# Kernel tuning notes

Measured on AMD Instinct MI355X. Metric: run time of the kernel, lower is better.

## Reference

```python
import jax, jax.numpy as jnp
import numpy as np

B, L, D, H, NE, M, NP, C, F2 = 2, 1024, 768, 12, 42, 8, 1722, 97, 256


def setup_inputs() -> dict:
    key = jax.random.key(0)
    ks = jax.random.split(key, 12)
    s = 0.02
    sequence_output = jax.random.normal(ks[0], (B, L, D), jnp.float32)
    attention = jax.random.uniform(ks[1], (B, H, L, L), jnp.float32)
    mention_idx = jax.random.randint(ks[2], (B, NE, M), 0, L)
    mention_mask = jax.random.randint(ks[3], (B, NE, M), 0, 2).at[:, :, 0].set(1)
    hts = jax.random.randint(ks[4], (B, NP, 2), 0, NE)
    return dict(
        sequence_output=sequence_output, attention=attention,
        mention_idx=mention_idx, mention_mask=mention_mask, hts=hts,
        W_lin=jax.random.normal(ks[5], (D, 3)) * s, b_lin=jnp.zeros((3,)),
        W_seg=jax.random.normal(ks[6], (3, F2)) * s, b_seg=jnp.zeros((F2,)),
        W_head=jax.random.normal(ks[7], (D, F2)) * s, b_head=jnp.zeros((F2,)),
        W_tail=jax.random.normal(ks[8], (D, F2)) * s, b_tail=jnp.zeros((F2,)),
        W_bil=jax.random.normal(ks[9], (C, F2, F2)) * s, b_bil=jnp.zeros((C,)),
    )


def reference(sequence_output, attention, mention_idx, mention_mask, hts,
              W_lin, b_lin, W_seg, b_seg, W_head, b_head, W_tail, b_tail,
              W_bil, b_bil):
    b_, l_, d_ = sequence_output.shape
    h_ = attention.shape[1]
    ne, m_ = mention_idx.shape[1:]
    NEG = jnp.asarray(-1e30, sequence_output.dtype)
    msk = mention_mask.astype(sequence_output.dtype)  # [B,NE,M]

    bidx = jnp.arange(b_)[:, None, None]
    # --- get_hrt: per-entity mention gather + logsumexp pool / mean pool ---
    ment_emb = sequence_output[bidx, mention_idx]              # [B,NE,M,D]
    ent_emb = jax.nn.logsumexp(jnp.where(msk[..., None] > 0, ment_emb, NEG), axis=2)  # [B,NE,D]
    ment_att = attention[bidx, :, mention_idx]                 # [B,NE,M,H,L]
    ent_att = (ment_att * msk[..., None, None]).sum(2) / msk.sum(2)[..., None, None]  # [B,NE,H,L]

    b2 = jnp.arange(b_)[:, None]
    hs = ent_emb[b2, hts[..., 0]]                              # [B,NP,D]
    ts = ent_emb[b2, hts[..., 1]]

    # --- get_channel_map: all ne*ne pair attention-weighted context ---
    hi = jnp.repeat(jnp.arange(ne), ne)
    ti = jnp.tile(jnp.arange(ne), ne)
    h_att = ent_att[:, hi]                                     # [B,NE*NE,H,L]
    t_att = ent_att[:, ti]
    ht_att = jnp.einsum('bphl,bphl->bpl', h_att, t_att) / h_   # mean over heads
    ht_att = ht_att / (ht_att.sum(-1, keepdims=True) + 1e-5)
    rs = jnp.einsum('bld,bpl->bpd', sequence_output, ht_att)   # [B,NE*NE,D]
    feature_map = rs.reshape(b_, ne, ne, d_)

    # self.linear (D->3) then segmentation net (stand-in: 1x1 conv 3->F2 + relu)
    attn_input = feature_map @ W_lin + b_lin                   # [B,NE,NE,3]
    attn_map = jax.nn.relu(attn_input @ W_seg + b_seg)         # [B,NE,NE,F2]

    # --- get_ht: gather pair features ---
    h_t = attn_map[b2, hts[..., 0], hts[..., 1]]               # [B,NP,F2]
    hs = jnp.tanh(hs @ W_head + b_head + h_t)
    ts = jnp.tanh(ts @ W_tail + b_tail + h_t)
    logits = jnp.einsum('bpi,oij,bpj->bpo', hs, W_bil, ts) + b_bil
    return logits.reshape(-1, logits.shape[-1])               # [B*NP, C]
```

## Files before the change

### kernel.cpp

```cpp
#include <hip/hip_runtime.h>
#include <hip/hip_bf16.h>
#include <math.h>

constexpr int BB = 2;
constexpr int LL = 1024;
constexpr int DD = 768;
constexpr int HH = 12;
constexpr int NEz = 42;
constexpr int MM = 8;
constexpr int NPp = 1722;
constexpr int CC = 97;
constexpr int FF = 256;
constexpr int PAIRS = NEz * NEz;
constexpr int TOTAL = BB * NPp;
constexpr int PT64 = (TOTAL + 63) / 64;

typedef float f32x4 __attribute__((ext_vector_type(4)));
typedef short bf16x8 __attribute__((ext_vector_type(8)));

__global__ void k_seqw(const float* __restrict__ seq, const float* __restrict__ Wl,
                       float* __restrict__ seqW) {
    int bl = blockIdx.x;
    int lane = threadIdx.x;
    const float* row = seq + (size_t)bl * DD;
    float a0 = 0.f, a1 = 0.f, a2 = 0.f;
    for (int d = lane; d < DD; d += 64) {
        float v = row[d];
        a0 += v * Wl[d * 3 + 0];
        a1 += v * Wl[d * 3 + 1];
        a2 += v * Wl[d * 3 + 2];
    }
    for (int off = 32; off; off >>= 1) {
        a0 += __shfl_down(a0, off);
        a1 += __shfl_down(a1, off);
        a2 += __shfl_down(a2, off);
    }
    if (lane == 0) {
        seqW[bl * 3 + 0] = a0;
        seqW[bl * 3 + 1] = a1;
        seqW[bl * 3 + 2] = a2;
    }
}

__global__ void k_ent_emb(const float* __restrict__ seq, const int* __restrict__ midx,
                          const int* __restrict__ mmask, float* __restrict__ ent_emb) {
    int be = blockIdx.x;
    int b = be / NEz;
    int tid = threadIdx.x;
    int idx[MM], msk[MM];
#pragma unroll
    for (int m = 0; m < MM; ++m) {
        idx[m] = midx[be * MM + m];
        msk[m] = mmask[be * MM + m];
    }
    const float* sb = seq + (size_t)b * LL * DD;
    for (int d = tid; d < DD; d += 256) {
        float v[MM];
        float mx = -1e30f;
#pragma unroll
        for (int m = 0; m < MM; ++m) {
            v[m] = msk[m] ? sb[(size_t)idx[m] * DD + d] : -1e30f;
            mx = fmaxf(mx, v[m]);
        }
        float s = 0.f;
#pragma unroll
        for (int m = 0; m < MM; ++m) s += expf(v[m] - mx);
        ent_emb[(size_t)be * DD + d] = mx + logf(s);
    }
}

__global__ void k_ent_att(const float* __restrict__ att, const int* __restrict__ midx,
                          const int* __restrict__ mmask, float* __restrict__ ea) {
    int beh = blockIdx.x;
    int h = beh % HH;
    int be = beh / HH;
    int b = be / NEz;
    int tid = threadIdx.x;
    int idx[MM], msk[MM];
    float msum = 0.f;
#pragma unroll
    for (int m = 0; m < MM; ++m) {
        idx[m] = midx[be * MM + m];
        msk[m] = mmask[be * MM + m];
        msum += (float)msk[m];
    }
    float inv = 1.f / msum;
    const float* ab = att + ((size_t)b * HH + h) * LL * LL;
#pragma unroll
    for (int li = 0; li < 4; ++li) {
        int l = tid + li * 256;
        float acc = 0.f;
#pragma unroll
        for (int m = 0; m < MM; ++m)
            if (msk[m]) acc += ab[(size_t)idx[m] * LL + l];
        ea[(size_t)beh * LL + l] = acc * inv;
    }
}

__global__ void k_pair(const float* __restrict__ ea, const float* __restrict__ seqW,
                       const float* __restrict__ Wseg, const float* __restrict__ bseg,
                       const float* __restrict__ blin, float* __restrict__ am) {
    int bp = blockIdx.x;
    int b = bp / PAIRS;
    int p = bp % PAIRS;
    int e1 = p / NEz, e2 = p % NEz;
    int tid = threadIdx.x;
    int lane = tid & 63, wid = tid >> 6;

    const float* ea1 = ea + ((size_t)(b * NEz + e1)) * HH * LL;
    const float* ea2 = ea + ((size_t)(b * NEz + e2)) * HH * LL;

    float myht[4];
    float lsum = 0.f;
#pragma unroll
    for (int li = 0; li < 4; ++li) {
        int l = tid + li * 256;
        float acc = 0.f;
#pragma unroll
        for (int h = 0; h < HH; ++h) acc += ea1[h * LL + l] * ea2[h * LL + l];
        acc *= (1.0f / HH);
        myht[li] = acc;
        lsum += acc;
    }
    __shared__ float red4[4];
    __shared__ float redz[3][4];
    for (int off = 32; off; off >>= 1) lsum += __shfl_down(lsum, off);
    if (lane == 0) red4[wid] = lsum;
    __syncthreads();
    float s = red4[0] + red4[1] + red4[2] + red4[3];
    float scale = 1.f / (s + 1e-5f);

    float z0 = 0.f, z1 = 0.f, z2 = 0.f;
#pragma unroll
    for (int li = 0; li < 4; ++li) {
        int l = tid + li * 256;
        float w = myht[li] * scale;
        const float* sw = seqW + ((size_t)b * LL + l) * 3;
        z0 += w * sw[0];
        z1 += w * sw[1];
        z2 += w * sw[2];
    }
    for (int off = 32; off; off >>= 1) {
        z0 += __shfl_down(z0, off);
        z1 += __shfl_down(z1, off);
        z2 += __shfl_down(z2, off);
    }
    if (lane == 0) { redz[0][wid] = z0; redz[1][wid] = z1; redz[2][wid] = z2; }
    __syncthreads();
    float ai0 = redz[0][0] + redz[0][1] + redz[0][2] + redz[0][3] + blin[0];
    float ai1 = redz[1][0] + redz[1][1] + redz[1][2] + redz[1][3] + blin[1];
    float ai2 = redz[2][0] + redz[2][1] + redz[2][2] + redz[2][3] + blin[2];
    float val = ai0 * Wseg[0 * FF + tid] + ai1 * Wseg[1 * FF + tid] +
                ai2 * Wseg[2 * FF + tid] + bseg[tid];
    am[(size_t)bp * FF + tid] = fmaxf(val, 0.f);
}

__global__ void k_ew(const float* __restrict__ ent_emb, const float* __restrict__ Wh,
                     const float* __restrict__ bh, const float* __restrict__ Wt,
                     const float* __restrict__ bt, float* __restrict__ EWh,
                     float* __restrict__ EWt) {
    int be = blockIdx.x;
    int tid = threadIdx.x;
    __shared__ float e[DD];
    for (int d = tid; d < DD; d += 256) e[d] = ent_emb[(size_t)be * DD + d];
    __syncthreads();
    float ah = bh[tid], at = bt[tid];
    for (int d = 0; d < DD; ++d) {
        float ev = e[d];
        ah += ev * Wh[d * FF + tid];
        at += ev * Wt[d * FF + tid];
    }
    EWh[(size_t)be * FF + tid] = ah;
    EWt[(size_t)be * FF + tid] = at;
}

__global__ void k_wt(const float* __restrict__ Wb, __hip_bfloat16* __restrict__ Wt) {
    int o = blockIdx.y;
    int ti = blockIdx.x >> 2;
    int tj = blockIdx.x & 3;
    int tid = threadIdx.x;
    int lane = tid & 63, quad = tid >> 6;
    __shared__ float t64[64][65];
    const float* src = Wb + (size_t)o * FF * FF;
#pragma unroll 4
    for (int i = 0; i < 16; ++i) {
        int kr = quad * 16 + i;
        t64[kr][lane] = src[(size_t)(ti * 64 + kr) * FF + tj * 64 + lane];
    }
    __syncthreads();
    __hip_bfloat16* dst = Wt + (size_t)o * FF * FF;
#pragma unroll 4
    for (int i = 0; i < 16; ++i) {
        int jr = quad * 16 + i;
        dst[(size_t)(tj * 64 + jr) * FF + ti * 64 + lane] = __float2bfloat16(t64[lane][jr]);
    }
}

__global__ void k_prep(const float* __restrict__ EWh, const float* __restrict__ EWt,
                       const float* __restrict__ am, const int* __restrict__ hts,
                       __hip_bfloat16* __restrict__ HSb, __hip_bfloat16* __restrict__ TSb) {
    int bp = blockIdx.x;
    int b = bp / NPp;
    int t = threadIdx.x;
    int e1 = hts[bp * 2 + 0];
    int e2 = hts[bp * 2 + 1];
    float htv = am[((size_t)b * PAIRS + e1 * NEz + e2) * FF + t];
    float hv = tanhf(EWh[(size_t)(b * NEz + e1) * FF + t] + htv);
    float tv = tanhf(EWt[(size_t)(b * NEz + e2) * FF + t] + htv);
    HSb[(size_t)bp * FF + t] = __float2bfloat16(hv);
    TSb[(size_t)bp * FF + t] = __float2bfloat16(tv);
}

__launch_bounds__(256)
__global__ void k_bil_mfma(const __hip_bfloat16* __restrict__ HSb,
                           const __hip_bfloat16* __restrict__ TSb,
                           const __hip_bfloat16* __restrict__ Wtb,
                           const float* __restrict__ bbil,
                           float* __restrict__ out) {
    int p0 = blockIdx.x * 64;
    int o = blockIdx.y;
    int tid = threadIdx.x;
    int lane = tid & 63, w = tid >> 6;
    int lg = lane >> 4;
    int lr = lane & 15;

    __shared__ __hip_bfloat16 Alds[64 * 256];
    __shared__ __hip_bfloat16 Blds[256 * 64];
    __shared__ float rowred[64][4];

    char* A_c = (char*)Alds;
    char* B_c = (char*)Blds;

#pragma unroll
    for (int it = 0; it < 8; ++it) {
        int u = tid + it * 256;
        int r = u >> 5;
        int k16 = u & 31;
        bf16x8 v = {0, 0, 0, 0, 0, 0, 0, 0};
        int p = p0 + r;
        if (p < TOTAL) v = *(const bf16x8*)(const void*)(HSb + (size_t)p * FF + k16 * 8);
        int byte = (r * 512 + k16 * 16) ^ ((r & 7) << 4);
        *(bf16x8*)(A_c + byte) = v;
    }

    f32x4 acc[4][4];
#pragma unroll
    for (int mi = 0; mi < 4; ++mi)
#pragma unroll
        for (int ni = 0; ni < 4; ++ni) acc[mi][ni] = (f32x4){0.f, 0.f, 0.f, 0.f};

    const __hip_bfloat16* Wo = Wtb + (size_t)o * FF * FF;

    for (int kc = 0; kc < 4; ++kc) {
#pragma unroll
        for (int it = 0; it < 8; ++it) {
            int u = tid + it * 256;
            int n = u >> 3;
            int k16 = u & 7;
            bf16x8 v = *(const bf16x8*)(const void*)(Wo + (size_t)n * FF + kc * 64 + k16 * 8);
            int byte = (n * 128 + k16 * 16) ^ ((n & 7) << 4);
            *(bf16x8*)(B_c + byte) = v;
        }
        __syncthreads();
#pragma unroll
        for (int ks = 0; ks < 2; ++ks) {
            bf16x8 af[4], bf[4];
#pragma unroll
            for (int mi = 0; mi < 4; ++mi) {
                int r = mi * 16 + lr;
                int k = kc * 64 + ks * 32 + lg * 8;
                int byte = (r * 512 + k * 2) ^ ((r & 7) << 4);
                af[mi] = *(const bf16x8*)(A_c + byte);
            }
#pragma unroll
            for (int ni = 0; ni < 4; ++ni) {
                int n = w * 64 + ni * 16 + lr;
                int k = ks * 32 + lg * 8;
                int byte = (n * 128 + k * 2) ^ ((n & 7) << 4);
                bf[ni] = *(const bf16x8*)(B_c + byte);
            }
#pragma unroll
            for (int mi = 0; mi < 4; ++mi)
#pragma unroll
                for (int ni = 0; ni < 4; ++ni)
                    acc[mi][ni] = __builtin_amdgcn_mfma_f32_16x16x32_bf16(
                        af[mi], bf[ni], acc[mi][ni], 0, 0, 0);
        }
        __syncthreads();
    }

#pragma unroll
    for (int it = 0; it < 8; ++it) {
        int u = tid + it * 256;
        int r = u >> 5;
        int k16 = u & 31;
        bf16x8 v = {0, 0, 0, 0, 0, 0, 0, 0};
        int p = p0 + r;
        if (p < TOTAL) v = *(const bf16x8*)(const void*)(TSb + (size_t)p * FF + k16 * 8);
        *(bf16x8*)(B_c + r * 512 + k16 * 16) = v;
    }
    __syncthreads();

    const unsigned short* TSl = (const unsigned short*)Blds;
#pragma unroll
    for (int mi = 0; mi < 4; ++mi) {
#pragma unroll
        for (int reg = 0; reg < 4; ++reg) {
            int r = mi * 16 + lg * 4 + reg;
            float s = 0.f;
#pragma unroll
            for (int ni = 0; ni < 4; ++ni) {
                int c = w * 64 + ni * 16 + lr;
                float tsv = __uint_as_float((unsigned)TSl[r * 256 + c] << 16);
                s += acc[mi][ni][reg] * tsv;
            }
            s += __shfl_xor(s, 1);
            s += __shfl_xor(s, 2);
            s += __shfl_xor(s, 4);
            s += __shfl_xor(s, 8);
            if (lr == 0) rowred[r][w] = s;
        }
    }
    __syncthreads();
    if (tid < 64) {
        int p = p0 + tid;
        if (p < TOTAL)
            out[(size_t)p * CC + o] = rowred[tid][0] + rowred[tid][1] +
                                      rowred[tid][2] + rowred[tid][3] + bbil[o];
    }
}

extern "C" void kernel_launch(void* const* d_in, const int* in_sizes, int n_in,
                              void* d_out, int out_size, void* d_ws, size_t ws_size,
                              hipStream_t stream) {
    const float* seq   = (const float*)d_in[0];
    const float* att   = (const float*)d_in[1];
    const int*   midx  = (const int*)d_in[2];
    const int*   mmask = (const int*)d_in[3];
    const int*   hts   = (const int*)d_in[4];
    const float* Wlin  = (const float*)d_in[5];
    const float* blin  = (const float*)d_in[6];
    const float* Wseg  = (const float*)d_in[7];
    const float* bseg  = (const float*)d_in[8];
    const float* Whead = (const float*)d_in[9];
    const float* bhead = (const float*)d_in[10];
    const float* Wtail = (const float*)d_in[11];
    const float* btail = (const float*)d_in[12];
    const float* Wbil  = (const float*)d_in[13];
    const float* bbil  = (const float*)d_in[14];
    float* out = (float*)d_out;

    float* ws = (float*)d_ws;
    float* ent_emb = ws;
    float* ea      = ent_emb + BB * NEz * DD;
    float* seqW    = ea + (size_t)BB * NEz * HH * LL;
    float* am      = seqW + BB * LL * 3;
    float* EWh     = am + (size_t)BB * PAIRS * FF;
    float* EWt     = EWh + BB * NEz * FF;
    __hip_bfloat16* Wtb = (__hip_bfloat16*)(EWt + BB * NEz * FF);
    __hip_bfloat16* HSb = Wtb + (size_t)CC * FF * FF;
    __hip_bfloat16* TSb = HSb + (size_t)TOTAL * FF;

    k_seqw<<<BB * LL, 64, 0, stream>>>(seq, Wlin, seqW);
    k_ent_emb<<<BB * NEz, 256, 0, stream>>>(seq, midx, mmask, ent_emb);
    k_ent_att<<<BB * NEz * HH, 256, 0, stream>>>(att, midx, mmask, ea);
    k_pair<<<BB * PAIRS, 256, 0, stream>>>(ea, seqW, Wseg, bseg, blin, am);
    k_ew<<<BB * NEz, 256, 0, stream>>>(ent_emb, Whead, bhead, Wtail, btail, EWh, EWt);
    k_wt<<<dim3(16, CC), 256, 0, stream>>>(Wbil, Wtb);
    k_prep<<<TOTAL, 256, 0, stream>>>(EWh, EWt, am, hts, HSb, TSb);
    k_bil_mfma<<<dim3(PT64, CC), 256, 0, stream>>>(HSb, TSb, Wtb, bbil, out);
}
```

Baseline: 195.1 us.

## Pre-swizzle bilinear operands, batch 8 outputs per block, double-buffer weight loads

The weight transpose and the HS preparation now write bf16 data already in the swizzled LDS layout, so the bilinear kernel can copy it straight into shared memory. Each 512-thread block handles a 64-pair tile for 8 output classes and keeps the HS tile resident in LDS. Weight chunks are prefetched into registers one chunk ahead, with hand-placed barriers and setprio around the MFMAs, and blocks are remapped across XCDs. TS values are held in registers and results are staged for a grouped store. The aim is to cut redundant HS reloads and hide global latency, at the cost of more register pressure and more complex synchronisation.

```diff
diff --git a/kernel.cpp b/kernel.cpp
--- a/kernel.cpp
+++ b/kernel.cpp
@@ -14,9 +14,17 @@
 constexpr int PAIRS = NEz * NEz;
 constexpr int TOTAL = BB * NPp;
 constexpr int PT64 = (TOTAL + 63) / 64;
+constexpr int OG = 8;
+constexpr int OGRP = (CC + OG - 1) / OG;
+constexpr int NWG = PT64 * OGRP;
 
 typedef float f32x4 __attribute__((ext_vector_type(4)));
 typedef short bf16x8 __attribute__((ext_vector_type(8)));
+
+__device__ inline short f2bs(float x) {
+    __hip_bfloat16 b = __float2bfloat16(x);
+    return *(short*)&b;
+}
 
 __global__ void k_seqw(const float* __restrict__ seq, const float* __restrict__ Wl,
                        float* __restrict__ seqW) {
@@ -188,146 +196,220 @@
         t64[kr][lane] = src[(size_t)(ti * 64 + kr) * FF + tj * 64 + lane];
     }
     __syncthreads();
-    __hip_bfloat16* dst = Wt + (size_t)o * FF * FF;
-#pragma unroll 4
-    for (int i = 0; i < 16; ++i) {
-        int jr = quad * 16 + i;
-        dst[(size_t)(tj * 64 + jr) * FF + ti * 64 + lane] = __float2bfloat16(t64[lane][jr]);
+    char* dst = (char*)Wt + (size_t)o * 131072 + (size_t)ti * 32768;
+#pragma unroll
+    for (int u2 = 0; u2 < 2; ++u2) {
+        int u = tid + u2 * 256;
+        int jr = u >> 3;
+        int k16 = u & 7;
+        int n = tj * 64 + jr;
+        bf16x8 val;
+#pragma unroll
+        for (int kk = 0; kk < 8; ++kk) val[kk] = f2bs(t64[k16 * 8 + kk][jr]);
+        *(bf16x8*)(dst + ((n * 128 + k16 * 16) ^ ((n & 7) << 4))) = val;
     }
 }
 
 __global__ void k_prep(const float* __restrict__ EWh, const float* __restrict__ EWt,
                        const float* __restrict__ am, const int* __restrict__ hts,
-                       __hip_bfloat16* __restrict__ HSb, __hip_bfloat16* __restrict__ TSb) {
-    int bp = blockIdx.x;
-    int b = bp / NPp;
-    int t = threadIdx.x;
-    int e1 = hts[bp * 2 + 0];
-    int e2 = hts[bp * 2 + 1];
-    float htv = am[((size_t)b * PAIRS + e1 * NEz + e2) * FF + t];
-    float hv = tanhf(EWh[(size_t)(b * NEz + e1) * FF + t] + htv);
-    float tv = tanhf(EWt[(size_t)(b * NEz + e2) * FF + t] + htv);
-    HSb[(size_t)bp * FF + t] = __float2bfloat16(hv);
-    TSb[(size_t)bp * FF + t] = __float2bfloat16(tv);
-}
-
-__launch_bounds__(256)
-__global__ void k_bil_mfma(const __hip_bfloat16* __restrict__ HSb,
+                       __hip_bfloat16* __restrict__ HS_swz, __hip_bfloat16* __restrict__ TSb) {
+    int tile = blockIdx.x;
+    int tid = threadIdx.x;
+    char* dstA = (char*)HS_swz + (size_t)tile * 32768;
+#pragma unroll
+    for (int u2 = 0; u2 < 8; ++u2) {
+        int u = tid + u2 * 256;
+        int r = u >> 5;
+        int k16 = u & 31;
+        int p = tile * 64 + r;
+        bf16x8 hv8 = {0, 0, 0, 0, 0, 0, 0, 0};
+        bf16x8 tv8 = {0, 0, 0, 0, 0, 0, 0, 0};
+        if (p < TOTAL) {
+            int b = p / NPp;
+            int e1 = hts[p * 2 + 0];
+            int e2 = hts[p * 2 + 1];
+            const float* amr = am + ((size_t)b * PAIRS + e1 * NEz + e2) * FF + k16 * 8;
+            const float* hr = EWh + (size_t)(b * NEz + e1) * FF + k16 * 8;
+            const float* tr = EWt + (size_t)(b * NEz + e2) * FF + k16 * 8;
+#pragma unroll
+            for (int kk = 0; kk < 8; ++kk) {
+                float a = amr[kk];
+                hv8[kk] = f2bs(tanhf(hr[kk] + a));
+                tv8[kk] = f2bs(tanhf(tr[kk] + a));
+            }
+            *(bf16x8*)((char*)TSb + (size_t)p * 512 + k16 * 16) = tv8;
+        }
+        *(bf16x8*)(dstA + ((r * 512 + k16 * 16) ^ ((r & 7) << 4))) = hv8;
+    }
+}
+
+#define SYNC_PROD() do { __builtin_amdgcn_sched_barrier(0); \
+    asm volatile("s_waitcnt lgkmcnt(0)" ::: "memory"); \
+    __builtin_amdgcn_sched_barrier(0); \
+    __builtin_amdgcn_s_barrier(); \
+    __builtin_amdgcn_sched_barrier(0); } while (0)
+#define SYNC_X() do { __builtin_amdgcn_sched_barrier(0); \
+    __builtin_amdgcn_s_barrier(); \
+    __builtin_amdgcn_sched_barrier(0); } while (0)
+
+__launch_bounds__(512, 4)
+__global__ void k_bil_mfma(const __hip_bfloat16* __restrict__ HS_swz,
                            const __hip_bfloat16* __restrict__ TSb,
-                           const __hip_bfloat16* __restrict__ Wtb,
+                           const __hip_bfloat16* __restrict__ Wt_swz,
                            const float* __restrict__ bbil,
                            float* __restrict__ out) {
-    int p0 = blockIdx.x * 64;
-    int o = blockIdx.y;
+    int f = blockIdx.x;
+    constexpr int Q = NWG / 8, R8 = NWG % 8;
+    int xcd = f & 7, sub = f >> 3;
+    int wg = (xcd < R8 ? xcd * (Q + 1) : R8 * (Q + 1) + (xcd - R8) * Q) + sub;
+    int og = wg / PT64;
+    int tile = wg % PT64;
+    int p0 = tile * 64;
+    int o0 = og * OG;
+    int nO = CC - o0 < OG ? CC - o0 : OG;
+
     int tid = threadIdx.x;
     int lane = tid & 63, w = tid >> 6;
-    int lg = lane >> 4;
-    int lr = lane & 15;
-
-    __shared__ __hip_bfloat16 Alds[64 * 256];
-    __shared__ __hip_bfloat16 Blds[256 * 64];
+    int wr = w >> 2, wc = w & 3;
+    int lr = lane & 15, lg = lane >> 4;
+
+    __shared__ char A_c[32768];
+    __shared__ char B_c[32768];
     __shared__ float rowred[64][4];
-
-    char* A_c = (char*)Alds;
-    char* B_c = (char*)Blds;
-
-#pragma unroll
-    for (int it = 0; it < 8; ++it) {
-        int u = tid + it * 256;
-        int r = u >> 5;
-        int k16 = u & 31;
-        bf16x8 v = {0, 0, 0, 0, 0, 0, 0, 0};
+    __shared__ float outbuf[64][OG];
+
+    bf16x8* Bv = (bf16x8*)B_c;
+    const bf16x8* Wu = (const bf16x8*)Wt_swz;
+
+    {
+        const bf16x8* Asrc = (const bf16x8*)(HS_swz) + (size_t)tile * 2048;
+        bf16x8* Av = (bf16x8*)A_c;
+#pragma unroll
+        for (int it = 0; it < 4; ++it) Av[tid + it * 512] = Asrc[tid + it * 512];
+    }
+
+    unsigned tsp[2][4][2];
+    {
+        const unsigned short* TSu = (const unsigned short*)TSb;
+#pragma unroll
+        for (int mi = 0; mi < 2; ++mi)
+#pragma unroll
+            for (int reg = 0; reg < 4; ++reg) {
+                int r = wr * 32 + mi * 16 + lg * 4 + reg;
+                int p = p0 + r;
+#pragma unroll
+                for (int np_ = 0; np_ < 2; ++np_) {
+                    unsigned lo = 0, hi = 0;
+                    if (p < TOTAL) {
+                        int c0 = wc * 64 + np_ * 32 + lr;
+                        lo = TSu[(size_t)p * FF + c0];
+                        hi = TSu[(size_t)p * FF + c0 + 16];
+                    }
+                    tsp[mi][reg][np_] = lo | (hi << 16);
+                }
+            }
+    }
+
+    int aoff[2], asw[2], boff[4], bsw[4];
+#pragma unroll
+    for (int mi = 0; mi < 2; ++mi) {
+        int r = wr * 32 + mi * 16 + lr;
+        aoff[mi] = r * 512;
+        asw[mi] = (r & 7) << 4;
+    }
+#pragma unroll
+    for (int ni = 0; ni < 4; ++ni) {
+        int n = wc * 64 + ni * 16 + lr;
+        boff[ni] = n * 128;
+        bsw[ni] = (n & 7) << 4;
+    }
+
+#define PREFETCH(PF, NX) do { \
+    const bf16x8* np_ = Wu + ((size_t)(o0 + ((NX) >> 2)) * 8192 + (size_t)((NX) & 3) * 2048); \
+    _Pragma("unroll") \
+    for (int it_ = 0; it_ < 4; ++it_) PF[it_] = np_[tid + it_ * 512]; \
+} while (0)
+
+#define WRITE_B(PF) do { \
+    _Pragma("unroll") \
+    for (int it_ = 0; it_ < 4; ++it_) Bv[tid + it_ * 512] = PF[it_]; \
+} while (0)
+
+#define COMPUTE(KC) do { \
+    _Pragma("unroll") \
+    for (int ks = 0; ks < 2; ++ks) { \
+        bf16x8 af[2], bfr[4]; \
+        int k2 = (KC) * 128 + ks * 64 + lg * 16; \
+        _Pragma("unroll") \
+        for (int mi = 0; mi < 2; ++mi) \
+            af[mi] = *(const bf16x8*)(A_c + (aoff[mi] + (k2 ^ asw[mi]))); \
+        int kk2 = ks * 64 + lg * 16; \
+        _Pragma("unroll") \
+        for (int ni = 0; ni < 4; ++ni) \
+            bfr[ni] = *(const bf16x8*)(B_c + (boff[ni] + (kk2 ^ bsw[ni]))); \
+        __builtin_amdgcn_s_setprio(1); \
+        _Pragma("unroll") \
+        for (int mi = 0; mi < 2; ++mi) \
+            _Pragma("unroll") \
+            for (int ni = 0; ni < 4; ++ni) \
+                acc[mi][ni] = __builtin_amdgcn_mfma_f32_16x16x32_bf16(af[mi], bfr[ni], acc[mi][ni], 0, 0, 0); \
+        __builtin_amdgcn_s_setprio(0); \
+    } \
+} while (0)
+
+    bf16x8 pfA[4], pfB[4];
+    PREFETCH(pfA, 0);
+
+    for (int oi = 0; oi < nO; ++oi) {
+        int lastc = nO * 4 - 1;
+        int nx1 = oi * 4 + 1; nx1 = nx1 > lastc ? lastc : nx1;
+        int nx2 = oi * 4 + 2; nx2 = nx2 > lastc ? lastc : nx2;
+        int nx3 = oi * 4 + 3; nx3 = nx3 > lastc ? lastc : nx3;
+        int nx4 = oi * 4 + 4; nx4 = nx4 > lastc ? lastc : nx4;
+
+        f32x4 acc[2][4];
+#pragma unroll
+        for (int mi = 0; mi < 2; ++mi)
+#pragma unroll
+            for (int ni = 0; ni < 4; ++ni) acc[mi][ni] = (f32x4){0.f, 0.f, 0.f, 0.f};
+
+        PREFETCH(pfB, nx1); SYNC_X(); WRITE_B(pfA); SYNC_PROD(); COMPUTE(0);
+        PREFETCH(pfA, nx2); SYNC_X(); WRITE_B(pfB); SYNC_PROD(); COMPUTE(1);
+        PREFETCH(pfB, nx3); SYNC_X(); WRITE_B(pfA); SYNC_PROD(); COMPUTE(2);
+        PREFETCH(pfA, nx4); SYNC_X(); WRITE_B(pfB); SYNC_PROD(); COMPUTE(3);
+
+#pragma unroll
+        for (int mi = 0; mi < 2; ++mi)
+#pragma unroll
+            for (int reg = 0; reg < 4; ++reg) {
+                unsigned u0 = tsp[mi][reg][0], u1 = tsp[mi][reg][1];
+                float t0 = __uint_as_float((u0 & 0xFFFFu) << 16);
+                float t1 = __uint_as_float(u0 & 0xFFFF0000u);
+                float t2 = __uint_as_float((u1 & 0xFFFFu) << 16);
+                float t3 = __uint_as_float(u1 & 0xFFFF0000u);
+                float s = acc[mi][0][reg] * t0 + acc[mi][1][reg] * t1 +
+                          acc[mi][2][reg] * t2 + acc[mi][3][reg] * t3;
+                s += __shfl_xor(s, 1);
+                s += __shfl_xor(s, 2);
+                s += __shfl_xor(s, 4);
+                s += __shfl_xor(s, 8);
+                if (lr == 0) rowred[wr * 32 + mi * 16 + lg * 4 + reg][wc] = s;
+            }
+        SYNC_PROD();
+        if (tid < 64)
+            outbuf[tid][oi] = rowred[tid][0] + rowred[tid][1] + rowred[tid][2] + rowred[tid][3];
+    }
+
+    SYNC_PROD();
+    {
+        int r = tid >> 3, oi2 = tid & 7;
         int p = p0 + r;
-        if (p < TOTAL) v = *(const bf16x8*)(const void*)(HSb + (size_t)p * FF + k16 * 8);
-        int byte = (r * 512 + k16 * 16) ^ ((r & 7) << 4);
-        *(bf16x8*)(A_c + byte) = v;
-    }
-
-    f32x4 acc[4][4];
-#pragma unroll
-    for (int mi = 0; mi < 4; ++mi)
-#pragma unroll
-        for (int ni = 0; ni < 4; ++ni) acc[mi][ni] = (f32x4){0.f, 0.f, 0.f, 0.f};
-
-    const __hip_bfloat16* Wo = Wtb + (size_t)o * FF * FF;
-
-    for (int kc = 0; kc < 4; ++kc) {
-#pragma unroll
-        for (int it = 0; it < 8; ++it) {
-            int u = tid + it * 256;
-            int n = u >> 3;
-            int k16 = u & 7;
-            bf16x8 v = *(const bf16x8*)(const void*)(Wo + (size_t)n * FF + kc * 64 + k16 * 8);
-            int byte = (n * 128 + k16 * 16) ^ ((n & 7) << 4);
-            *(bf16x8*)(B_c + byte) = v;
-        }
-        __syncthreads();
-#pragma unroll
-        for (int ks = 0; ks < 2; ++ks) {
-            bf16x8 af[4], bf[4];
-#pragma unroll
-            for (int mi = 0; mi < 4; ++mi) {
-                int r = mi * 16 + lr;
-                int k = kc * 64 + ks * 32 + lg * 8;
-                int byte = (r * 512 + k * 2) ^ ((r & 7) << 4);
-                af[mi] = *(const bf16x8*)(A_c + byte);
-            }
-#pragma unroll
-            for (int ni = 0; ni < 4; ++ni) {
-                int n = w * 64 + ni * 16 + lr;
-                int k = ks * 32 + lg * 8;
-                int byte = (n * 128 + k * 2) ^ ((n & 7) << 4);
-                bf[ni] = *(const bf16x8*)(B_c + byte);
-            }
-#pragma unroll
-            for (int mi = 0; mi < 4; ++mi)
-#pragma unroll
-                for (int ni = 0; ni < 4; ++ni)
-                    acc[mi][ni] = __builtin_amdgcn_mfma_f32_16x16x32_bf16(
-                        af[mi], bf[ni], acc[mi][ni], 0, 0, 0);
-        }
-        __syncthreads();
-    }
-
-#pragma unroll
-    for (int it = 0; it < 8; ++it) {
-        int u = tid + it * 256;
-        int r = u >> 5;
-        int k16 = u & 31;
-        bf16x8 v = {0, 0, 0, 0, 0, 0, 0, 0};
-        int p = p0 + r;
-        if (p < TOTAL) v = *(const bf16x8*)(const void*)(TSb + (size_t)p * FF + k16 * 8);
-        *(bf16x8*)(B_c + r * 512 + k16 * 16) = v;
-    }
-    __syncthreads();
-
-    const unsigned short* TSl = (const unsigned short*)Blds;
-#pragma unroll
-    for (int mi = 0; mi < 4; ++mi) {
-#pragma unroll
-        for (int reg = 0; reg < 4; ++reg) {
-            int r = mi * 16 + lg * 4 + reg;
-            float s = 0.f;
-#pragma unroll
-            for (int ni = 0; ni < 4; ++ni) {
-                int c = w * 64 + ni * 16 + lr;
-                float tsv = __uint_as_float((unsigned)TSl[r * 256 + c] << 16);
-                s += acc[mi][ni][reg] * tsv;
-            }
-            s += __shfl_xor(s, 1);
-            s += __shfl_xor(s, 2);
-            s += __shfl_xor(s, 4);
-            s += __shfl_xor(s, 8);
-            if (lr == 0) rowred[r][w] = s;
-        }
-    }
-    __syncthreads();
-    if (tid < 64) {
-        int p = p0 + tid;
-        if (p < TOTAL)
-            out[(size_t)p * CC + o] = rowred[tid][0] + rowred[tid][1] +
-                                      rowred[tid][2] + rowred[tid][3] + bbil[o];
-    }
+        if (oi2 < nO && p < TOTAL)
+            out[(size_t)p * CC + o0 + oi2] = outbuf[r][oi2] + bbil[o0 + oi2];
+    }
+#undef PREFETCH
+#undef WRITE_B
+#undef COMPUTE
 }
 
 extern "C" void kernel_launch(void* const* d_in, const int* in_sizes, int n_in,
@@ -357,16 +439,16 @@
     float* am      = seqW + BB * LL * 3;
     float* EWh     = am + (size_t)BB * PAIRS * FF;
     float* EWt     = EWh + BB * NEz * FF;
-    __hip_bfloat16* Wtb = (__hip_bfloat16*)(EWt + BB * NEz * FF);
-    __hip_bfloat16* HSb = Wtb + (size_t)CC * FF * FF;
-    __hip_bfloat16* TSb = HSb + (size_t)TOTAL * FF;
+    __hip_bfloat16* Wt_swz = (__hip_bfloat16*)(EWt + BB * NEz * FF);
+    __hip_bfloat16* HS_swz = Wt_swz + (size_t)CC * FF * FF;
+    __hip_bfloat16* TSb    = HS_swz + (size_t)PT64 * 64 * FF;
 
     k_seqw<<<BB * LL, 64, 0, stream>>>(seq, Wlin, seqW);
     k_ent_emb<<<BB * NEz, 256, 0, stream>>>(seq, midx, mmask, ent_emb);
     k_ent_att<<<BB * NEz * HH, 256, 0, stream>>>(att, midx, mmask, ea);
     k_pair<<<BB * PAIRS, 256, 0, stream>>>(ea, seqW, Wseg, bseg, blin, am);
     k_ew<<<BB * NEz, 256, 0, stream>>>(ent_emb, Whead, bhead, Wtail, btail, EWh, EWt);
-    k_wt<<<dim3(16, CC), 256, 0, stream>>>(Wbil, Wtb);
-    k_prep<<<TOTAL, 256, 0, stream>>>(EWh, EWt, am, hts, HSb, TSb);
-    k_bil_mfma<<<dim3(PT64, CC), 256, 0, stream>>>(HSb, TSb, Wtb, bbil, out);
-}
+    k_wt<<<dim3(16, CC), 256, 0, stream>>>(Wbil, Wt_swz);
+    k_prep<<<PT64, 256, 0, stream>>>(EWh, EWt, am, hts, HS_swz, TSb);
+    k_bil_mfma<<<NWG, 512, 0, stream>>>(HS_swz, TSb, Wt_swz, bbil, out);
+}
```

Result: slower. 203.4 us (+4.2%).
